# Performance work log

Hardware: AMD Instinct MI355X
Metric: run time of the kernel (lower is better)

## Reference

```python
import jax, jax.numpy as jnp
from jax import lax
import numpy as np

NUM_LABELS = 48
BATCH, SEQ_LEN = 512, 1024


def setup_inputs() -> dict:
    key = jax.random.key(0)
    k1, k2, k3, k4, k5 = jax.random.split(key, 5)
    emissions = jax.random.normal(k1, (BATCH, SEQ_LEN, NUM_LABELS), dtype=jnp.float32)
    labels = jax.random.randint(k2, (BATCH, SEQ_LEN), 0, NUM_LABELS, dtype=jnp.int32)
    mask = jnp.ones((BATCH, SEQ_LEN), dtype=jnp.int32)
    transitions = jax.random.normal(k3, (NUM_LABELS, NUM_LABELS), dtype=jnp.float32)
    start_transitions = jax.random.normal(k4, (NUM_LABELS,), dtype=jnp.float32)
    end_transitions = jax.random.normal(k5, (NUM_LABELS,), dtype=jnp.float32)
    return {
        "emissions": emissions,
        "labels": labels,
        "mask": mask,
        "transitions": transitions,
        "start_transitions": start_transitions,
        "end_transitions": end_transitions,
    }


def _gold_score(emissions, labels, mask, transitions, start_transitions, end_transitions):
    maskf = mask.astype(emissions.dtype)
    # emissions gathered at gold labels: (B, T)
    emit = jnp.take_along_axis(emissions, labels[..., None], axis=2)[..., 0]
    # NOTE: original indexes transitions[labels_t, labels_{t-1}] (cur, prev)
    trans = transitions[labels[:, 1:], labels[:, :-1]]  # (B, T-1)
    lengths = jnp.sum(mask, axis=1) - 1  # index of last real token
    last_labels = jnp.take_along_axis(labels, lengths[:, None], axis=1)[:, 0]
    score = (start_transitions[labels[:, 0]] + emit[:, 0]
             + jnp.sum((emit[:, 1:] + trans) * maskf[:, 1:], axis=1)
             + end_transitions[last_labels])
    return score  # (B,)


def _forward_algorithm(emissions, mask, transitions, start_transitions, end_transitions):
    # carry: alpha scores (B, L)
    score0 = start_transitions[None, :] + emissions[:, 0]

    def step(score, xs):
        emit_t, mask_t = xs  # (B, L), (B,)
        # logsumexp over previous label i of score[b,i] + transitions[i,j]
        next_score = jax.nn.logsumexp(score[:, :, None] + transitions[None, :, :], axis=1) + emit_t
        score = jnp.where(mask_t[:, None].astype(bool), next_score, score)
        return score, None

    xs = (jnp.moveaxis(emissions[:, 1:], 1, 0), jnp.moveaxis(mask[:, 1:], 1, 0))
    score, _ = lax.scan(step, score0, xs)
    return jax.nn.logsumexp(score + end_transitions[None, :], axis=1)  # (B,)


def reference(emissions, labels, mask, transitions, start_transitions, end_transitions):
    gold = _gold_score(emissions, labels, mask, transitions, start_transitions, end_transitions)
    fwd = _forward_algorithm(emissions, mask, transitions, start_transitions, end_transitions)
    return jnp.mean(fwd - gold)
```

## Files before the change

kernel.cpp:

```cpp
#include <hip/hip_runtime.h>

constexpr int NL    = 48;
constexpr int SEQ   = 1024;
constexpr int BATCH = 512;

__device__ __forceinline__ float lane_bcast(float v, int lane) {
    return __int_as_float(__builtin_amdgcn_readlane(__float_as_int(v), lane));
}

#define CRF_STEP(T_, SLOT_, RN_) do {                                         \
    float ee_ = __expf(embuf[SLOT_]);                                         \
    int   mt_ = mbuf[SLOT_];                                                  \
    int   tn_ = (T_) + 8; if (tn_ > SEQ - 1) tn_ = SEQ - 1;                   \
    embuf[SLOT_] = em[tn_ * NL + jc];                                         \
    mbuf[SLOT_]  = mk[tn_];                                                   \
    float sv_[NL];                                                            \
    _Pragma("unroll")                                                         \
    for (int i_ = 0; i_ < NL; ++i_) sv_[i_] = lane_bcast(v, i_);              \
    float rm_ = 1.0f;                                                         \
    if (RN_) {                                                                \
        unsigned um_ = __float_as_uint(sv_[0]);                               \
        _Pragma("unroll")                                                     \
        for (int i_ = 1; i_ < NL; ++i_) {                                     \
            unsigned u2_ = __float_as_uint(sv_[i_]);                          \
            um_ = (um_ > u2_) ? um_ : u2_;                                    \
        }                                                                     \
        float m_ = __uint_as_float(um_);                                      \
        rm_ = __builtin_amdgcn_rcpf(m_);                                      \
        S += __logf(m_);                                                      \
    }                                                                         \
    float a0_ = 0.f, a1_ = 0.f, a2_ = 0.f, a3_ = 0.f;                         \
    _Pragma("unroll")                                                         \
    for (int i_ = 0; i_ < NL; i_ += 4) {                                      \
        a0_ = fmaf(sv_[i_ + 0], Ec[i_ + 0], a0_);                             \
        a1_ = fmaf(sv_[i_ + 1], Ec[i_ + 1], a1_);                             \
        a2_ = fmaf(sv_[i_ + 2], Ec[i_ + 2], a2_);                             \
        a3_ = fmaf(sv_[i_ + 3], Ec[i_ + 3], a3_);                             \
    }                                                                         \
    float acc_ = (a0_ + a1_) + (a2_ + a3_);                                   \
    v = (mt_ ? acc_ * ee_ : v) * rm_;                                         \
} while (0)

__global__ __launch_bounds__(128)
__attribute__((amdgpu_waves_per_eu(1, 1)))
void crf_fused(
    const float* __restrict__ emissions, const int* __restrict__ labels,
    const int* __restrict__ mask, const float* __restrict__ trans,
    const float* __restrict__ startt, const float* __restrict__ endt,
    float* __restrict__ gold_out, float* __restrict__ fwd_out)
{
    const int b   = blockIdx.x;
    const int tid = threadIdx.x;
    const float* em = emissions + (size_t)b * SEQ * NL;
    const int*   mk = mask + b * SEQ;

    if (tid < 64) {
        const int  j   = tid;
        const bool act = (j < NL);
        const int  jc  = act ? j : NL - 1;

        float Ec[NL];
        #pragma unroll
        for (int i = 0; i < NL; ++i) Ec[i] = __expf(trans[i * NL + jc]);

        float s0 = act ? (startt[jc] + em[jc]) : -3.0e38f;
        float m0 = s0;
        #pragma unroll
        for (int o = 32; o; o >>= 1) m0 = fmaxf(m0, __shfl_xor(m0, o));
        float v = act ? __expf(s0 - m0) : 0.0f;
        float S = m0;

        float embuf[8]; int mbuf[8];
        #pragma unroll
        for (int t = 1; t <= 8; ++t) { embuf[t & 7] = em[t * NL + jc]; mbuf[t & 7] = mk[t]; }

        CRF_STEP(1, 1, 0); CRF_STEP(2, 2, 0); CRF_STEP(3, 3, 0); CRF_STEP(4, 4, 0);
        CRF_STEP(5, 5, 1); CRF_STEP(6, 6, 0); CRF_STEP(7, 7, 0);

        for (int tb = 8; tb <= SEQ - 8; tb += 8) {
            CRF_STEP(tb + 0, 0, 1);
            CRF_STEP(tb + 1, 1, 0); CRF_STEP(tb + 2, 2, 0); CRF_STEP(tb + 3, 3, 0);
            CRF_STEP(tb + 4, 4, 1);
            CRF_STEP(tb + 5, 5, 0); CRF_STEP(tb + 6, 6, 0); CRF_STEP(tb + 7, 7, 0);
        }

        float w = act ? v * __expf(endt[jc]) : 0.0f;
        #pragma unroll
        for (int o = 32; o; o >>= 1) w += __shfl_xor(w, o);
        if (j == 0) fwd_out[b] = S + __logf(w);
    } else {
        const int l = tid - 64;
        const int* lb = labels + b * SEQ;

        float part = 0.0f; int mcnt = 0;
        for (int t = l; t < SEQ; t += 64) {
            int lt = lb[t];
            int mt = mk[t];
            mcnt += mt;
            if (t == 0) {
                part += startt[lt] + em[lt];
            } else {
                float e  = em[t * NL + lt];
                float tr = trans[lt * NL + lb[t - 1]];
                if (mt) part += e + tr;
            }
        }
        #pragma unroll
        for (int o = 32; o; o >>= 1) {
            part += __shfl_xor(part, o);
            mcnt += __shfl_xor(mcnt, o);
        }
        if (l == 0) {
            int len = mcnt - 1;
            gold_out[b] = part + endt[lb[len]];
        }
    }
}

__global__ __launch_bounds__(64) void crf_reduce(
    const float* __restrict__ gold, const float* __restrict__ fwd,
    float* __restrict__ out)
{
    const int l = threadIdx.x;
    float s = 0.0f;
    for (int bIdx = l; bIdx < BATCH; bIdx += 64) s += fwd[bIdx] - gold[bIdx];
    #pragma unroll
    for (int o = 32; o; o >>= 1) s += __shfl_xor(s, o);
    if (l == 0) out[0] = s * (1.0f / (float)BATCH);
}

extern "C" void kernel_launch(void* const* d_in, const int* in_sizes, int n_in,
                              void* d_out, int out_size, void* d_ws, size_t ws_size,
                              hipStream_t stream) {
    const float* emissions = (const float*)d_in[0];
    const int*   labels    = (const int*)d_in[1];
    const int*   mask      = (const int*)d_in[2];
    const float* trans     = (const float*)d_in[3];
    const float* startt    = (const float*)d_in[4];
    const float* endt      = (const float*)d_in[5];
    float*       out       = (float*)d_out;
    float*       wsf       = (float*)d_ws;

    crf_fused<<<BATCH, 128, 0, stream>>>(emissions, labels, mask, trans, startt, endt,
                                         wsf, wsf + BATCH);
    crf_reduce<<<1, 64, 0, stream>>>(wsf, wsf + BATCH, out);
}
```

Measured before the change: 358.6 us.

## Broadcast alpha via LDS with packed FMAs and ballot-packed mask bits

Each step of the forward recurrence now writes the alpha vector to a 64-float shared buffer and reads it back as float4 broadcasts. This replaces 48 per-lane readlane broadcasts. The dot product uses 2-wide packed FMAs over pre-paired exp(transitions). Per-step mask loads become one bitmask per 8 steps built with a wave ballot. The renormalisation max is now a shuffle-xor reduction instead of a scan over the broadcast values. This trades scalar readlane traffic for LDS round-trip latency on the serial critical path, and relies on single-wave ordering without a barrier.

```diff
diff --git a/kernel.cpp b/kernel.cpp
--- a/kernel.cpp
+++ b/kernel.cpp
@@ -4,41 +4,41 @@
 constexpr int SEQ   = 1024;
 constexpr int BATCH = 512;
 
-__device__ __forceinline__ float lane_bcast(float v, int lane) {
-    return __int_as_float(__builtin_amdgcn_readlane(__float_as_int(v), lane));
+typedef float f2 __attribute__((ext_vector_type(2)));
+typedef float f4 __attribute__((ext_vector_type(4)));
+
+__device__ __forceinline__ f2 fma2(f2 a, f2 b, f2 c) {
+    return __builtin_elementwise_fma(a, b, c);
 }
 
 #define CRF_STEP(T_, SLOT_, RN_) do {                                         \
     float ee_ = __expf(embuf[SLOT_]);                                         \
-    int   mt_ = mbuf[SLOT_];                                                  \
+    int   mt_ = (int)((mb_cur >> (SLOT_)) & 1);                               \
     int   tn_ = (T_) + 8; if (tn_ > SEQ - 1) tn_ = SEQ - 1;                   \
     embuf[SLOT_] = em[tn_ * NL + jc];                                         \
-    mbuf[SLOT_]  = mk[tn_];                                                   \
-    float sv_[NL];                                                            \
-    _Pragma("unroll")                                                         \
-    for (int i_ = 0; i_ < NL; ++i_) sv_[i_] = lane_bcast(v, i_);              \
     float rm_ = 1.0f;                                                         \
     if (RN_) {                                                                \
-        unsigned um_ = __float_as_uint(sv_[0]);                               \
+        float m_ = v;                                                         \
         _Pragma("unroll")                                                     \
-        for (int i_ = 1; i_ < NL; ++i_) {                                     \
-            unsigned u2_ = __float_as_uint(sv_[i_]);                          \
-            um_ = (um_ > u2_) ? um_ : u2_;                                    \
-        }                                                                     \
-        float m_ = __uint_as_float(um_);                                      \
+        for (int o_ = 32; o_; o_ >>= 1) m_ = fmaxf(m_, __shfl_xor(m_, o_));   \
         rm_ = __builtin_amdgcn_rcpf(m_);                                      \
         S += __logf(m_);                                                      \
     }                                                                         \
-    float a0_ = 0.f, a1_ = 0.f, a2_ = 0.f, a3_ = 0.f;                         \
+    f2 c0_ = {0.f, 0.f}, c1_ = {0.f, 0.f};                                    \
+    f2 c2_ = {0.f, 0.f}, c3_ = {0.f, 0.f};                                    \
     _Pragma("unroll")                                                         \
-    for (int i_ = 0; i_ < NL; i_ += 4) {                                      \
-        a0_ = fmaf(sv_[i_ + 0], Ec[i_ + 0], a0_);                             \
-        a1_ = fmaf(sv_[i_ + 1], Ec[i_ + 1], a1_);                             \
-        a2_ = fmaf(sv_[i_ + 2], Ec[i_ + 2], a2_);                             \
-        a3_ = fmaf(sv_[i_ + 3], Ec[i_ + 3], a3_);                             \
+    for (int g_ = 0; g_ < 12; g_ += 2) {                                      \
+        f4 s_ = svl4[g_];                                                     \
+        c0_ = fma2(s_.xy, Ec2[2 * g_    ], c0_);                              \
+        c1_ = fma2(s_.zw, Ec2[2 * g_ + 1], c1_);                              \
+        f4 t_ = svl4[g_ + 1];                                                 \
+        c2_ = fma2(t_.xy, Ec2[2 * g_ + 2], c2_);                              \
+        c3_ = fma2(t_.zw, Ec2[2 * g_ + 3], c3_);                              \
     }                                                                         \
-    float acc_ = (a0_ + a1_) + (a2_ + a3_);                                   \
+    f2 cs_ = (c0_ + c2_) + (c1_ + c3_);                                       \
+    float acc_ = cs_.x + cs_.y;                                               \
     v = (mt_ ? acc_ * ee_ : v) * rm_;                                         \
+    svl[tid] = v;                                                             \
 } while (0)
 
 __global__ __launch_bounds__(128)
@@ -54,14 +54,26 @@
     const float* em = emissions + (size_t)b * SEQ * NL;
     const int*   mk = mask + b * SEQ;
 
+    __shared__ alignas(16) float svl[64];
+
     if (tid < 64) {
         const int  j   = tid;
         const bool act = (j < NL);
         const int  jc  = act ? j : NL - 1;
+        const f4*  svl4 = reinterpret_cast<const f4*>(svl);
 
-        float Ec[NL];
+        f2 Ec2[24];
         #pragma unroll
-        for (int i = 0; i < NL; ++i) Ec[i] = __expf(trans[i * NL + jc]);
+        for (int k = 0; k < 24; ++k) {
+            f2 e_;
+            e_.x = __expf(trans[(2 * k    ) * NL + jc]);
+            e_.y = __expf(trans[(2 * k + 1) * NL + jc]);
+            Ec2[k] = e_;
+        }
+
+        int mval = mk[tid & 7];
+        unsigned long long mb_cur = __ballot(mval != 0);
+        mval = mk[8 + (tid & 7)];
 
         float s0 = act ? (startt[jc] + em[jc]) : -3.0e38f;
         float m0 = s0;
@@ -69,15 +81,20 @@
         for (int o = 32; o; o >>= 1) m0 = fmaxf(m0, __shfl_xor(m0, o));
         float v = act ? __expf(s0 - m0) : 0.0f;
         float S = m0;
+        svl[tid] = v;
 
-        float embuf[8]; int mbuf[8];
+        float embuf[8];
         #pragma unroll
-        for (int t = 1; t <= 8; ++t) { embuf[t & 7] = em[t * NL + jc]; mbuf[t & 7] = mk[t]; }
+        for (int t = 1; t <= 8; ++t) embuf[t & 7] = em[t * NL + jc];
 
         CRF_STEP(1, 1, 0); CRF_STEP(2, 2, 0); CRF_STEP(3, 3, 0); CRF_STEP(4, 4, 0);
         CRF_STEP(5, 5, 1); CRF_STEP(6, 6, 0); CRF_STEP(7, 7, 0);
 
         for (int tb = 8; tb <= SEQ - 8; tb += 8) {
+            mb_cur = __ballot(mval != 0);
+            int tm = tb + 8 + (tid & 7);
+            if (tm > SEQ - 1) tm = SEQ - 1;
+            mval = mk[tm];
             CRF_STEP(tb + 0, 0, 1);
             CRF_STEP(tb + 1, 1, 0); CRF_STEP(tb + 2, 2, 0); CRF_STEP(tb + 3, 3, 0);
             CRF_STEP(tb + 4, 4, 1);
```

Result: faster. 324.0 us (-9.7%).
